# Optimization experiments

Measured on AMD Instinct MI355X. Metric: run time of the kernel, lower is better.

The kernel has to match this reference:

```python
import jax, jax.numpy as jnp
import numpy as np

SCALE = 32 ** (-0.5)  # hardcoded in the original module, independent of head_size

def setup_inputs() -> dict:
    key = jax.random.key(0)
    k1, k2, k3, k4 = jax.random.split(key, 4)
    B, T, E, H = 8, 4096, 2048, 128
    x = jax.random.normal(k1, (B, T, E), dtype=jnp.float32)
    Wq = jax.random.normal(k2, (E, H), dtype=jnp.float32) * (E ** -0.5)
    Wk = jax.random.normal(k3, (E, H), dtype=jnp.float32) * (E ** -0.5)
    Wv = jax.random.normal(k4, (E, H), dtype=jnp.float32) * (E ** -0.5)
    return {"x": x, "Wq": Wq, "Wk": Wk, "Wv": Wv}

def reference(x, Wq, Wk, Wv):
    # q,k,v: [B,T,H]
    q = jnp.einsum('bte,eh->bth', x, Wq)
    k = jnp.einsum('bte,eh->bth', x, Wk)
    v = jnp.einsum('bte,eh->bth', x, Wv)
    # wei: [B, T(query), T(key)]
    wei = jnp.einsum('bqh,bkh->bqk', q, k) * SCALE
    # NOTE: original uses F.softmax(wei, dim=1) -> normalize over the QUERY axis
    wei = jax.nn.softmax(wei, axis=1)
    # dropout prob is 0 in this deterministic baseline (eval mode)
    out = jnp.einsum('bqk,bkh->bqh', wei, v)
    return out
```

## Files before the change

kernel.cpp:

```cpp
#include <hip/hip_runtime.h>
#include <hip/hip_bf16.h>
#include <hip/hip_fp16.h>

#define Bn 8
#define Tn 4096
#define En 2048
#define Hn 128

typedef __attribute__((ext_vector_type(8))) short bf16x8;
typedef __attribute__((ext_vector_type(4))) float f32x4;
typedef __attribute__((ext_vector_type(4))) unsigned int u32x4;

typedef const __attribute__((address_space(1))) unsigned int* gptr_t;
typedef __attribute__((address_space(3))) unsigned int* lptr_t;

static __device__ __forceinline__ void gload16(const void* g, void* l) {
    __builtin_amdgcn_global_load_lds((gptr_t)g, (lptr_t)l, 16, 0, 0);
}

static __device__ __forceinline__ unsigned short f2bf(float f) {
    union { float f; unsigned u; } v; v.f = f;
    unsigned r = v.u + 0x7FFFu + ((v.u >> 16) & 1u);
    return (unsigned short)(r >> 16);
}

#define MFMA16(a, b, c) __builtin_amdgcn_mfma_f32_16x16x32_bf16((a), (b), (c), 0, 0, 0)
#define EXP2F(x) __builtin_amdgcn_exp2f(x)

__global__ __launch_bounds__(256) void conv_x(const float* __restrict__ x,
                                              unsigned short* __restrict__ xb) {
    size_t i = ((size_t)blockIdx.x * 256 + threadIdx.x) * 8;
    float4 a = *reinterpret_cast<const float4*>(x + i);
    float4 b = *reinterpret_cast<const float4*>(x + i + 4);
    ushort4 o0, o1;
    o0.x = f2bf(a.x); o0.y = f2bf(a.y); o0.z = f2bf(a.z); o0.w = f2bf(a.w);
    o1.x = f2bf(b.x); o1.y = f2bf(b.y); o1.z = f2bf(b.z); o1.w = f2bf(b.w);
    *reinterpret_cast<ushort4*>(xb + i) = o0;
    *reinterpret_cast<ushort4*>(xb + i + 4) = o1;
}

__global__ __launch_bounds__(256) void prep_w(const float* __restrict__ Wq,
                                              const float* __restrict__ Wk,
                                              const float* __restrict__ Wv,
                                              unsigned short* __restrict__ Wt) {
    int idx = blockIdx.x * 256 + threadIdx.x;
    int w = idx / (En * Hn);
    int rem = idx - w * (En * Hn);
    int kx = rem >> 7;
    int n  = rem & 127;
    const float* W = (w == 0) ? Wq : (w == 1) ? Wk : Wv;
    float f = W[rem];
    if (w == 0) f *= (0.17677669529663687f * 1.4426950408889634f);
    Wt[(size_t)w * En * Hn + (size_t)n * En + kx] = f2bf(f);
}

__global__ __launch_bounds__(256, 3) void qkv_mfma(const unsigned short* __restrict__ xb,
                                                   const unsigned short* __restrict__ Wt,
                                                   unsigned short* __restrict__ qs,
                                                   unsigned short* __restrict__ ks,
                                                   unsigned short* __restrict__ vT) {
    __shared__ unsigned short Al[128][64];
    __shared__ unsigned short Bl[128][64];
    const int bid = blockIdx.x;
    const int w = bid % 3;
    const int m0 = (bid / 3) * 128;
    const int b = m0 >> 12;
    const int tb = m0 & (Tn - 1);
    const int t = threadIdx.x;
    const int lane = t & 63, wid = t >> 6;
    const int wr = (wid >> 1) * 64, wc = (wid & 1) * 64;
    const int fr = lane & 15, fq = lane >> 4;
    const unsigned short* Wb = Wt + (size_t)w * En * Hn;
    const int sr = lane >> 3, sc = lane & 7;

    f32x4 acc[4][4] = {};
    for (int k0 = 0; k0 < En; k0 += 64) {
        __syncthreads();
        #pragma unroll
        for (int s = 0; s < 4; ++s) {
            int seg = wid * 4 + s;
            int r = seg * 8 + sr;
            gload16(&xb[(size_t)(m0 + r) * En + k0 + sc * 8],
                    (char*)&Al[0][0] + seg * 1024 + lane * 16);
            gload16(&Wb[(size_t)r * En + k0 + sc * 8],
                    (char*)&Bl[0][0] + seg * 1024 + lane * 16);
        }
        __syncthreads();
        #pragma unroll
        for (int ksub = 0; ksub < 2; ++ksub) {
            bf16x8 av[4], bv[4];
            #pragma unroll
            for (int mi = 0; mi < 4; ++mi)
                av[mi] = *reinterpret_cast<const bf16x8*>(&Al[wr + mi * 16 + fr][ksub * 32 + fq * 8]);
            #pragma unroll
            for (int ni = 0; ni < 4; ++ni)
                bv[ni] = *reinterpret_cast<const bf16x8*>(&Bl[wc + ni * 16 + fr][ksub * 32 + fq * 8]);
            #pragma unroll
            for (int mi = 0; mi < 4; ++mi)
                #pragma unroll
                for (int ni = 0; ni < 4; ++ni)
                    acc[mi][ni] = MFMA16(av[mi], bv[ni], acc[mi][ni]);
        }
    }

    if (w < 2) {
        unsigned short* out = (w == 0) ? qs : ks;
        #pragma unroll
        for (int mi = 0; mi < 4; ++mi)
            #pragma unroll
            for (int ni = 0; ni < 4; ++ni)
                #pragma unroll
                for (int r = 0; r < 4; ++r) {
                    int row = m0 + wr + mi * 16 + fq * 4 + r;
                    int col = wc + ni * 16 + fr;
                    out[(size_t)row * Hn + col] = f2bf(acc[mi][ni][r]);
                }
    } else {
        #pragma unroll
        for (int mi = 0; mi < 4; ++mi)
            #pragma unroll
            for (int ni = 0; ni < 4; ++ni)
                #pragma unroll
                for (int r = 0; r < 4; ++r) {
                    int tt = tb + wr + mi * 16 + fq * 4 + r;
                    int h  = wc + ni * 16 + fr;
                    vT[((size_t)b * Hn + h) * Tn + tt] = f2bf(acc[mi][ni][r]);
                }
    }
}

__global__ __launch_bounds__(256, 4) void stats_qk(const unsigned short* __restrict__ qs,
                                                   const unsigned short* __restrict__ ks,
                                                   float2* __restrict__ part) {
    __shared__ __align__(16) unsigned short Kl[64][128];
    __shared__ __align__(16) unsigned short Ql[64][128];
    const int bid = blockIdx.x;
    const int b = bid >> 7;
    const int kt = (bid >> 1) & 63;
    const int qh = bid & 1;
    const int k0 = kt * 64;
    const unsigned short* qb = qs + (size_t)b * Tn * Hn;
    const unsigned short* kb = ks + (size_t)b * Tn * Hn;
    const int t = threadIdx.x;
    const int lane = t & 63, wid = t >> 6;
    const int wk = wid >> 1, wq = wid & 1;
    const int fr = lane & 15, fq = lane >> 4;
    const int srow = t >> 4, schk = t & 15;

    #pragma unroll
    for (int it = 0; it < 4; ++it) {
        int r = it * 16 + srow;
        gload16(&kb[(size_t)(k0 + r) * Hn + ((schk ^ (r & 15)) * 8)],
                (char*)&Kl[0][0] + it * 4096 + t * 16);
    }
    __syncthreads();
    bf16x8 av[2][4];
    #pragma unroll
    for (int mi = 0; mi < 2; ++mi)
        #pragma unroll
        for (int kc = 0; kc < 4; ++kc) {
            int row = wk * 32 + mi * 16 + fr;
            int ch = (kc * 4 + fq) ^ (row & 15);
            av[mi][kc] = *reinterpret_cast<const bf16x8*>((const char*)Kl + row * 256 + ch * 16);
        }

    float m[2][4], l[2][4];
    #pragma unroll
    for (int mi = 0; mi < 2; ++mi)
        #pragma unroll
        for (int r = 0; r < 4; ++r) { m[mi][r] = -INFINITY; l[mi][r] = 0.f; }

    for (int step = 0; step < 32; ++step) {
        const int q0 = qh * 2048 + step * 64;
        #pragma unroll
        for (int it = 0; it < 4; ++it) {
            int r = it * 16 + srow;
            gload16(&qb[(size_t)(q0 + r) * Hn + ((schk ^ (r & 15)) * 8)],
                    (char*)&Ql[0][0] + it * 4096 + t * 16);
        }
        __syncthreads();
        f32x4 acc[2][2] = {};
        #pragma unroll
        for (int kc = 0; kc < 4; ++kc) {
            bf16x8 bv[2];
            #pragma unroll
            for (int ni = 0; ni < 2; ++ni) {
                int row = wq * 32 + ni * 16 + fr;
                int ch = (kc * 4 + fq) ^ (row & 15);
                bv[ni] = *reinterpret_cast<const bf16x8*>((const char*)Ql + row * 256 + ch * 16);
            }
            #pragma unroll
            for (int mi = 0; mi < 2; ++mi)
                #pragma unroll
                for (int ni = 0; ni < 2; ++ni)
                    acc[mi][ni] = MFMA16(av[mi][kc], bv[ni], acc[mi][ni]);
        }
        #pragma unroll
        for (int mi = 0; mi < 2; ++mi)
            #pragma unroll
            for (int r = 0; r < 4; ++r) {
                float v0 = acc[mi][0][r], v1 = acc[mi][1][r];
                float mn = fmaxf(m[mi][r], fmaxf(v0, v1));
                l[mi][r] = l[mi][r] * EXP2F(m[mi][r] - mn) + EXP2F(v0 - mn) + EXP2F(v1 - mn);
                m[mi][r] = mn;
            }
        __syncthreads();
    }
    #pragma unroll
    for (int off = 1; off <= 8; off <<= 1) {
        #pragma unroll
        for (int mi = 0; mi < 2; ++mi)
            #pragma unroll
            for (int r = 0; r < 4; ++r) {
                float mo = __shfl_xor(m[mi][r], off);
                float lo = __shfl_xor(l[mi][r], off);
                float mn = fmaxf(m[mi][r], mo);
                l[mi][r] = l[mi][r] * EXP2F(m[mi][r] - mn) + lo * EXP2F(mo - mn);
                m[mi][r] = mn;
            }
    }
    if (fr == 0) {
        #pragma unroll
        for (int mi = 0; mi < 2; ++mi)
            #pragma unroll
            for (int r = 0; r < 4; ++r) {
                int k = k0 + wk * 32 + mi * 16 + fq * 4 + r;
                part[((size_t)b * Tn + k) * 4 + qh * 2 + wq] = make_float2(m[mi][r], l[mi][r]);
            }
    }
}

__global__ __launch_bounds__(256) void stats_comb(const float2* __restrict__ part,
                                                  float* __restrict__ mr) {
    int g = blockIdx.x * 256 + threadIdx.x;
    const float2* pp = part + (size_t)g * 4;
    float2 p0 = pp[0], p1 = pp[1], p2 = pp[2], p3 = pp[3];
    float M = fmaxf(fmaxf(p0.x, p1.x), fmaxf(p2.x, p3.x));
    float L = p0.y * EXP2F(p0.x - M) + p1.y * EXP2F(p1.x - M) +
              p2.y * EXP2F(p2.x - M) + p3.y * EXP2F(p3.x - M);
    mr[g] = M + __log2f(L);
}

__global__ __launch_bounds__(256, 2) void attn_pv(const unsigned short* __restrict__ qs,
                                                  const unsigned short* __restrict__ ks,
                                                  const unsigned short* __restrict__ vT,
                                                  const float* __restrict__ mr,
                                                  float* __restrict__ out) {
    __shared__ __align__(16) char smem[73728];
    char* Qb = smem;
    char* Kb = smem + 16384;
    char* Vb2 = smem + 32768;
    char* Pb = smem + 65536;
    const int bid = blockIdx.x;
    const int b = bid >> 6;
    const int q0 = (bid & 63) * 64;
    const unsigned short* qg = qs + (size_t)b * Tn * Hn;
    const unsigned short* kg = ks + (size_t)b * Tn * Hn;
    const unsigned short* vg = vT + (size_t)b * Hn * Tn;
    const float* mrb = mr + (size_t)b * Tn;
    const int t = threadIdx.x;
    const int lane = t & 63, wid = t >> 6;
    const int wk = wid >> 1, wq = wid & 1;
    const int fr = lane & 15, fq = lane >> 4;
    const int srow16 = t >> 4, schk16 = t & 15;
    const int srow8 = t >> 3, schk8 = t & 7;

    #pragma unroll
    for (int it = 0; it < 4; ++it) {
        int r = it * 16 + srow16;
        gload16(&qg[(size_t)(q0 + r) * Hn + ((schk16 ^ (r & 15)) * 8)], Qb + it * 4096 + t * 16);
        gload16(&kg[(size_t)r * Hn + ((schk16 ^ (r & 15)) * 8)], Kb + it * 4096 + t * 16);
        int rv = it * 32 + srow8;
        gload16(&vg[(size_t)rv * Tn + ((schk8 ^ (rv & 7)) * 8)], Vb2 + it * 4096 + t * 16);
    }
    __syncthreads();
    bf16x8 bq[2][4];
    #pragma unroll
    for (int ni = 0; ni < 2; ++ni)
        #pragma unroll
        for (int kc = 0; kc < 4; ++kc) {
            int row = wq * 32 + ni * 16 + fr;
            int ch = (kc * 4 + fq) ^ (row & 15);
            bq[ni][kc] = *reinterpret_cast<const bf16x8*>(Qb + row * 256 + ch * 16);
        }

    f32x4 acc_o[4][2] = {};
    for (int kt = 0; kt < 64; ++kt) {
        const int k0 = kt * 64;
        f32x4 acc_s[2][2] = {};
        #pragma unroll
        for (int kc = 0; kc < 4; ++kc) {
            bf16x8 avk[2];
            #pragma unroll
            for (int mi = 0; mi < 2; ++mi) {
                int row = wk * 32 + mi * 16 + fr;
                int ch = (kc * 4 + fq) ^ (row & 15);
                avk[mi] = *reinterpret_cast<const bf16x8*>(Kb + row * 256 + ch * 16);
            }
            #pragma unroll
            for (int mi = 0; mi < 2; ++mi)
                #pragma unroll
                for (int ni = 0; ni < 2; ++ni)
                    acc_s[mi][ni] = MFMA16(avk[mi], bq[ni][kc], acc_s[mi][ni]);
        }
        #pragma unroll
        for (int mi = 0; mi < 2; ++mi) {
            float4 mk = *reinterpret_cast<const float4*>(&mrb[k0 + wk * 32 + mi * 16 + fq * 4]);
            #pragma unroll
            for (int ni = 0; ni < 2; ++ni) {
                unsigned p01 = (unsigned)f2bf(EXP2F(acc_s[mi][ni][0] - mk.x)) |
                               ((unsigned)f2bf(EXP2F(acc_s[mi][ni][1] - mk.y)) << 16);
                unsigned p23 = (unsigned)f2bf(EXP2F(acc_s[mi][ni][2] - mk.z)) |
                               ((unsigned)f2bf(EXP2F(acc_s[mi][ni][3] - mk.w)) << 16);
                int q = wq * 32 + ni * 16 + fr;
                int chunk = (wk * 4 + mi * 2 + (fq >> 1)) ^ (q & 7);
                *reinterpret_cast<uint2*>(Pb + q * 128 + chunk * 16 + (fq & 1) * 8) =
                    make_uint2(p01, p23);
            }
        }
        __syncthreads();
        if (kt < 63) {
            const int kn = k0 + 64;
            #pragma unroll
            for (int it = 0; it < 4; ++it) {
                int r = it * 16 + srow16;
                gload16(&kg[(size_t)(kn + r) * Hn + ((schk16 ^ (r & 15)) * 8)],
                        Kb + it * 4096 + t * 16);
                int rv = it * 32 + srow8;
                gload16(&vg[(size_t)rv * Tn + kn + ((schk8 ^ (rv & 7)) * 8)],
                        Vb2 + ((kt + 1) & 1) * 16384 + it * 4096 + t * 16);
            }
        }
        const char* Vcur = Vb2 + (kt & 1) * 16384;
        #pragma unroll
        for (int kc = 0; kc < 2; ++kc) {
            bf16x8 bp[2];
            #pragma unroll
            for (int ni = 0; ni < 2; ++ni) {
                int qrow = wq * 32 + ni * 16 + fr;
                int ch = (kc * 4 + fq) ^ (qrow & 7);
                bp[ni] = *reinterpret_cast<const bf16x8*>(Pb + qrow * 128 + ch * 16);
            }
            #pragma unroll
            for (int mi = 0; mi < 4; ++mi) {
                int row = wk * 64 + mi * 16 + fr;
                int ch = (kc * 4 + fq) ^ (row & 7);
                bf16x8 avv = *reinterpret_cast<const bf16x8*>(Vcur + row * 128 + ch * 16);
                #pragma unroll
                for (int ni = 0; ni < 2; ++ni)
                    acc_o[mi][ni] = MFMA16(avv, bp[ni], acc_o[mi][ni]);
            }
        }
        __syncthreads();
    }

    float* Ol = (float*)smem;
    #pragma unroll
    for (int mi = 0; mi < 4; ++mi)
        #pragma unroll
        for (int ni = 0; ni < 2; ++ni) {
            int q = wq * 32 + ni * 16 + fr;
            int h = wk * 64 + mi * 16 + fq * 4;
            *reinterpret_cast<float4*>(&Ol[q * 132 + h]) =
                make_float4(acc_o[mi][ni][0], acc_o[mi][ni][1], acc_o[mi][ni][2], acc_o[mi][ni][3]);
        }
    __syncthreads();
    #pragma unroll
    for (int j = 0; j < 8; ++j) {
        int idx = j * 256 + t;
        int row = idx >> 5, c = (idx & 31) * 4;
        *reinterpret_cast<float4*>(&out[((size_t)b * Tn + q0 + row) * Hn + c]) =
            *reinterpret_cast<const float4*>(&Ol[row * 132 + c]);
    }
}

extern "C" void kernel_launch(void* const* d_in, const int* in_sizes, int n_in,
                              void* d_out, int out_size, void* d_ws, size_t ws_size,
                              hipStream_t stream) {
    const float* x  = (const float*)d_in[0];
    const float* Wq = (const float*)d_in[1];
    const float* Wk = (const float*)d_in[2];
    const float* Wv = (const float*)d_in[3];
    float* out = (float*)d_out;

    char* p = (char*)d_ws;
    unsigned short* qs = (unsigned short*)p; p += (size_t)Bn * Tn * Hn * 2;
    unsigned short* ks = (unsigned short*)p; p += (size_t)Bn * Tn * Hn * 2;
    unsigned short* vT = (unsigned short*)p; p += (size_t)Bn * Tn * Hn * 2;
    unsigned short* Wt = (unsigned short*)p; p += (size_t)3 * En * Hn * 2;
    unsigned short* xb = (unsigned short*)p; p += (size_t)Bn * Tn * En * 2;
    float2* part       = (float2*)p;         p += (size_t)Bn * Tn * 4 * sizeof(float2);
    float* mr          = (float*)p;          p += (size_t)Bn * Tn * sizeof(float);
    size_t needed = (size_t)(p - (char*)d_ws);
    if (ws_size < needed) return;

    conv_x<<<dim3(Bn * Tn * En / (256 * 8)), dim3(256), 0, stream>>>(x, xb);
    prep_w<<<dim3(3 * En * Hn / 256), dim3(256), 0, stream>>>(Wq, Wk, Wv, Wt);
    qkv_mfma<<<dim3((Bn * Tn / 128) * 3), dim3(256), 0, stream>>>(xb, Wt, qs, ks, vT);
    stats_qk<<<dim3(Bn * 64 * 2), dim3(256), 0, stream>>>(qs, ks, part);
    stats_comb<<<dim3(Bn * Tn / 256), dim3(256), 0, stream>>>(part, mr);
    attn_pv<<<dim3(Bn * 64), dim3(256), 0, stream>>>(qs, ks, vT, mr, out);
}
```

Baseline: 295.0 us.

## Double-buffer Q/K/V tiles with vmcnt-based barriers and MFMA priority in attention kernels

stats_qk now double-buffers the Q tile in shared memory and prefetches the next tile before computing the current one. attn_pv double-buffers K alongside V, loads Q fragments straight from global into registers, and hoists the row-stat loads. Both kernels swap __syncthreads for explicit vmcnt/lgkmcnt waits plus s_barrier and raise wave priority around the MFMA blocks, so global loads overlap with compute. stats_qk's launch bound drops from 4 to 3 blocks per CU to fit the larger shared footprint, which may lower occupancy. The last iteration issues a redundant wrap-around prefetch.

```diff
diff --git a/kernel.cpp b/kernel.cpp
--- a/kernel.cpp
+++ b/kernel.cpp
@@ -26,6 +26,13 @@
 
 #define MFMA16(a, b, c) __builtin_amdgcn_mfma_f32_16x16x32_bf16((a), (b), (c), 0, 0, 0)
 #define EXP2F(x) __builtin_amdgcn_exp2f(x)
+#define WAIT_VM_PUB(N) do { asm volatile("s_waitcnt vmcnt(" #N ")" ::: "memory"); \
+                            __builtin_amdgcn_sched_barrier(0); \
+                            __builtin_amdgcn_s_barrier(); \
+                            __builtin_amdgcn_sched_barrier(0); } while (0)
+#define LGKM_BARRIER() do { asm volatile("s_waitcnt lgkmcnt(0)" ::: "memory"); \
+                            __builtin_amdgcn_s_barrier(); \
+                            __builtin_amdgcn_sched_barrier(0); } while (0)
 
 __global__ __launch_bounds__(256) void conv_x(const float* __restrict__ x,
                                               unsigned short* __restrict__ xb) {
@@ -129,11 +136,10 @@
     }
 }
 
-__global__ __launch_bounds__(256, 4) void stats_qk(const unsigned short* __restrict__ qs,
+__global__ __launch_bounds__(256, 3) void stats_qk(const unsigned short* __restrict__ qs,
                                                    const unsigned short* __restrict__ ks,
                                                    float2* __restrict__ part) {
-    __shared__ __align__(16) unsigned short Kl[64][128];
-    __shared__ __align__(16) unsigned short Ql[64][128];
+    __shared__ __align__(16) char smem[49152];
     const int bid = blockIdx.x;
     const int b = bid >> 7;
     const int kt = (bid >> 1) & 63;
@@ -151,7 +157,9 @@
     for (int it = 0; it < 4; ++it) {
         int r = it * 16 + srow;
         gload16(&kb[(size_t)(k0 + r) * Hn + ((schk ^ (r & 15)) * 8)],
-                (char*)&Kl[0][0] + it * 4096 + t * 16);
+                smem + it * 4096 + t * 16);
+        gload16(&qb[(size_t)(qh * 2048 + r) * Hn + ((schk ^ (r & 15)) * 8)],
+                smem + 16384 + it * 4096 + t * 16);
     }
     __syncthreads();
     bf16x8 av[2][4];
@@ -161,7 +169,7 @@
         for (int kc = 0; kc < 4; ++kc) {
             int row = wk * 32 + mi * 16 + fr;
             int ch = (kc * 4 + fq) ^ (row & 15);
-            av[mi][kc] = *reinterpret_cast<const bf16x8*>((const char*)Kl + row * 256 + ch * 16);
+            av[mi][kc] = *reinterpret_cast<const bf16x8*>(smem + row * 256 + ch * 16);
         }
 
     float m[2][4], l[2][4];
@@ -171,15 +179,18 @@
         for (int r = 0; r < 4; ++r) { m[mi][r] = -INFINITY; l[mi][r] = 0.f; }
 
     for (int step = 0; step < 32; ++step) {
-        const int q0 = qh * 2048 + step * 64;
+        const int cur = step & 1;
+        const int qn = qh * 2048 + ((step + 1) & 31) * 64;
         #pragma unroll
         for (int it = 0; it < 4; ++it) {
             int r = it * 16 + srow;
-            gload16(&qb[(size_t)(q0 + r) * Hn + ((schk ^ (r & 15)) * 8)],
-                    (char*)&Ql[0][0] + it * 4096 + t * 16);
-        }
-        __syncthreads();
+            gload16(&qb[(size_t)(qn + r) * Hn + ((schk ^ (r & 15)) * 8)],
+                    smem + 16384 + (cur ^ 1) * 16384 + it * 4096 + t * 16);
+        }
+        WAIT_VM_PUB(4);
+        const char* Qc = smem + 16384 + cur * 16384;
         f32x4 acc[2][2] = {};
+        __builtin_amdgcn_s_setprio(1);
         #pragma unroll
         for (int kc = 0; kc < 4; ++kc) {
             bf16x8 bv[2];
@@ -187,7 +198,7 @@
             for (int ni = 0; ni < 2; ++ni) {
                 int row = wq * 32 + ni * 16 + fr;
                 int ch = (kc * 4 + fq) ^ (row & 15);
-                bv[ni] = *reinterpret_cast<const bf16x8*>((const char*)Ql + row * 256 + ch * 16);
+                bv[ni] = *reinterpret_cast<const bf16x8*>(Qc + row * 256 + ch * 16);
             }
             #pragma unroll
             for (int mi = 0; mi < 2; ++mi)
@@ -195,6 +206,7 @@
                 for (int ni = 0; ni < 2; ++ni)
                     acc[mi][ni] = MFMA16(av[mi][kc], bv[ni], acc[mi][ni]);
         }
+        __builtin_amdgcn_s_setprio(0);
         #pragma unroll
         for (int mi = 0; mi < 2; ++mi)
             #pragma unroll
@@ -204,7 +216,7 @@
                 l[mi][r] = l[mi][r] * EXP2F(m[mi][r] - mn) + EXP2F(v0 - mn) + EXP2F(v1 - mn);
                 m[mi][r] = mn;
             }
-        __syncthreads();
+        LGKM_BARRIER();
     }
     #pragma unroll
     for (int off = 1; off <= 8; off <<= 1) {
@@ -247,9 +259,6 @@
                                                   const float* __restrict__ mr,
                                                   float* __restrict__ out) {
     __shared__ __align__(16) char smem[73728];
-    char* Qb = smem;
-    char* Kb = smem + 16384;
-    char* Vb2 = smem + 32768;
     char* Pb = smem + 65536;
     const int bid = blockIdx.x;
     const int b = bid >> 6;
@@ -265,29 +274,47 @@
     const int srow16 = t >> 4, schk16 = t & 15;
     const int srow8 = t >> 3, schk8 = t & 7;
 
+    bf16x8 bq[2][4];
+    #pragma unroll
+    for (int ni = 0; ni < 2; ++ni)
+        #pragma unroll
+        for (int kc = 0; kc < 4; ++kc) {
+            int row = q0 + wq * 32 + ni * 16 + fr;
+            bq[ni][kc] = *reinterpret_cast<const bf16x8*>(&qg[(size_t)row * Hn + kc * 32 + fq * 8]);
+        }
     #pragma unroll
     for (int it = 0; it < 4; ++it) {
         int r = it * 16 + srow16;
-        gload16(&qg[(size_t)(q0 + r) * Hn + ((schk16 ^ (r & 15)) * 8)], Qb + it * 4096 + t * 16);
-        gload16(&kg[(size_t)r * Hn + ((schk16 ^ (r & 15)) * 8)], Kb + it * 4096 + t * 16);
+        gload16(&kg[(size_t)r * Hn + ((schk16 ^ (r & 15)) * 8)], smem + it * 4096 + t * 16);
         int rv = it * 32 + srow8;
-        gload16(&vg[(size_t)rv * Tn + ((schk8 ^ (rv & 7)) * 8)], Vb2 + it * 4096 + t * 16);
+        gload16(&vg[(size_t)rv * Tn + ((schk8 ^ (rv & 7)) * 8)],
+                smem + 32768 + it * 4096 + t * 16);
     }
     __syncthreads();
-    bf16x8 bq[2][4];
-    #pragma unroll
-    for (int ni = 0; ni < 2; ++ni)
-        #pragma unroll
-        for (int kc = 0; kc < 4; ++kc) {
-            int row = wq * 32 + ni * 16 + fr;
-            int ch = (kc * 4 + fq) ^ (row & 15);
-            bq[ni][kc] = *reinterpret_cast<const bf16x8*>(Qb + row * 256 + ch * 16);
-        }
 
     f32x4 acc_o[4][2] = {};
     for (int kt = 0; kt < 64; ++kt) {
+        const int cur = kt & 1;
         const int k0 = kt * 64;
+        float4 mk0 = *reinterpret_cast<const float4*>(&mrb[k0 + wk * 32 + fq * 4]);
+        float4 mk1 = *reinterpret_cast<const float4*>(&mrb[k0 + wk * 32 + 16 + fq * 4]);
+        __builtin_amdgcn_sched_barrier(0);
+        {
+            const int knr = ((kt + 1) & 63) * 64;
+            #pragma unroll
+            for (int it = 0; it < 4; ++it) {
+                int r = it * 16 + srow16;
+                gload16(&kg[(size_t)(knr + r) * Hn + ((schk16 ^ (r & 15)) * 8)],
+                        smem + (cur ^ 1) * 16384 + it * 4096 + t * 16);
+                int rv = it * 32 + srow8;
+                gload16(&vg[(size_t)rv * Tn + knr + ((schk8 ^ (rv & 7)) * 8)],
+                        smem + 32768 + (cur ^ 1) * 16384 + it * 4096 + t * 16);
+            }
+        }
+        WAIT_VM_PUB(8);
+        const char* Kc = smem + cur * 16384;
         f32x4 acc_s[2][2] = {};
+        __builtin_amdgcn_s_setprio(1);
         #pragma unroll
         for (int kc = 0; kc < 4; ++kc) {
             bf16x8 avk[2];
@@ -295,7 +322,7 @@
             for (int mi = 0; mi < 2; ++mi) {
                 int row = wk * 32 + mi * 16 + fr;
                 int ch = (kc * 4 + fq) ^ (row & 15);
-                avk[mi] = *reinterpret_cast<const bf16x8*>(Kb + row * 256 + ch * 16);
+                avk[mi] = *reinterpret_cast<const bf16x8*>(Kc + row * 256 + ch * 16);
             }
             #pragma unroll
             for (int mi = 0; mi < 2; ++mi)
@@ -303,9 +330,10 @@
                 for (int ni = 0; ni < 2; ++ni)
                     acc_s[mi][ni] = MFMA16(avk[mi], bq[ni][kc], acc_s[mi][ni]);
         }
+        __builtin_amdgcn_s_setprio(0);
         #pragma unroll
         for (int mi = 0; mi < 2; ++mi) {
-            float4 mk = *reinterpret_cast<const float4*>(&mrb[k0 + wk * 32 + mi * 16 + fq * 4]);
+            float4 mk = mi ? mk1 : mk0;
             #pragma unroll
             for (int ni = 0; ni < 2; ++ni) {
                 unsigned p01 = (unsigned)f2bf(EXP2F(acc_s[mi][ni][0] - mk.x)) |
@@ -318,20 +346,9 @@
                     make_uint2(p01, p23);
             }
         }
-        __syncthreads();
-        if (kt < 63) {
-            const int kn = k0 + 64;
-            #pragma unroll
-            for (int it = 0; it < 4; ++it) {
-                int r = it * 16 + srow16;
-                gload16(&kg[(size_t)(kn + r) * Hn + ((schk16 ^ (r & 15)) * 8)],
-                        Kb + it * 4096 + t * 16);
-                int rv = it * 32 + srow8;
-                gload16(&vg[(size_t)rv * Tn + kn + ((schk8 ^ (rv & 7)) * 8)],
-                        Vb2 + ((kt + 1) & 1) * 16384 + it * 4096 + t * 16);
-            }
-        }
-        const char* Vcur = Vb2 + (kt & 1) * 16384;
+        LGKM_BARRIER();
+        const char* Vc = smem + 32768 + cur * 16384;
+        __builtin_amdgcn_s_setprio(1);
         #pragma unroll
         for (int kc = 0; kc < 2; ++kc) {
             bf16x8 bp[2];
@@ -345,16 +362,18 @@
             for (int mi = 0; mi < 4; ++mi) {
                 int row = wk * 64 + mi * 16 + fr;
                 int ch = (kc * 4 + fq) ^ (row & 7);
-                bf16x8 avv = *reinterpret_cast<const bf16x8*>(Vcur + row * 128 + ch * 16);
+                bf16x8 avv = *reinterpret_cast<const bf16x8*>(Vc + row * 128 + ch * 16);
                 #pragma unroll
                 for (int ni = 0; ni < 2; ++ni)
                     acc_o[mi][ni] = MFMA16(avv, bp[ni], acc_o[mi][ni]);
             }
         }
-        __syncthreads();
+        __builtin_amdgcn_s_setprio(0);
+        LGKM_BARRIER();
     }
 
     float* Ol = (float*)smem;
+    __syncthreads();
     #pragma unroll
     for (int mi = 0; mi < 4; ++mi)
         #pragma unroll
```

New measurement: 296.1 us. Within noise of the previous version (+0.4%).
